# Kernel tuning notes

Measured on AMD Instinct MI355X. Metric: run time of the kernel, lower is better.

Reference implementation:

```python
import jax, jax.numpy as jnp
import numpy as np

VOCAB, INPUT, HIDDEN = 50000, 512, 1024
BATCH, MAX_LEN = 64, 256


def setup_inputs() -> dict:
    key = jax.random.key(0)
    ks = jax.random.split(key, 16)
    s = 0.02
    return {
        "last_output": jax.random.randint(ks[0], (BATCH,), 0, VOCAB),
        "last_hidden": jax.random.normal(ks[1], (BATCH, HIDDEN), jnp.float32),
        "encoder_outputs": jax.random.normal(ks[2], (MAX_LEN, BATCH, HIDDEN), jnp.float32),
        # embedding table (padding_idx=0 just means row 0 is a pad row; math is a plain gather)
        "embedding": jax.random.uniform(ks[3], (VOCAB, INPUT), jnp.float32, -0.25, 0.25),
        # concat attention: Linear(2H -> H) and v [H]
        "attn_W": jax.random.normal(ks[4], (HIDDEN, 2 * HIDDEN), jnp.float32) * s,
        "attn_b": jnp.zeros((HIDDEN,), jnp.float32),
        "v": jax.random.normal(ks[5], (HIDDEN,), jnp.float32) * s,
        # GRU (single layer): input size = INPUT + HIDDEN, gate order r,z,n (torch order)
        "W_ih": jax.random.normal(ks[6], (3 * HIDDEN, INPUT + HIDDEN), jnp.float32) * s,
        "W_hh": jax.random.uniform(ks[7], (3 * HIDDEN, HIDDEN), jnp.float32, -0.01, 0.01),
        "b_ih": jnp.zeros((3 * HIDDEN,), jnp.float32),
        "b_hh": jnp.zeros((3 * HIDDEN,), jnp.float32),
        # output projection Linear(2H -> vocab)
        "out_W": jax.random.normal(ks[8], (VOCAB, 2 * HIDDEN), jnp.float32) * s,
        "out_b": jnp.zeros((VOCAB,), jnp.float32),
    }


def reference(last_output, last_hidden, encoder_outputs, embedding,
              attn_W, attn_b, v, W_ih, W_hh, b_ih, b_hh, out_W, out_b):
    T, B, H = encoder_outputs.shape
    # --- embedding lookup: [B, INPUT]
    emb = embedding[last_output]

    # --- concat (Bahdanau-style, no tanh in original) attention, vectorized over T
    hid = jnp.broadcast_to(last_hidden[None], (T, B, H))
    cat = jnp.concatenate([hid, encoder_outputs], axis=-1)          # [T,B,2H]
    energy = jnp.einsum('tbk,hk->tbh', cat, attn_W) + attn_b        # [T,B,H]
    scores = jnp.einsum('tbh,h->bt', energy, v)                     # [B,T]
    attn = jax.nn.softmax(scores, axis=1)                           # [B,T]

    # --- context: [B,H]
    context = jnp.einsum('bt,tbh->bh', attn, encoder_outputs)

    # --- single GRU step (torch gate order r,z,n)
    x = jnp.concatenate([emb, context], axis=-1)                    # [B, INPUT+H]
    gi = x @ W_ih.T + b_ih                                          # [B,3H]
    gh = last_hidden @ W_hh.T + b_hh                                # [B,3H]
    i_r, i_z, i_n = jnp.split(gi, 3, axis=-1)
    h_r, h_z, h_n = jnp.split(gh, 3, axis=-1)
    r = jax.nn.sigmoid(i_r + h_r)
    z = jax.nn.sigmoid(i_z + h_z)
    n = jnp.tanh(i_n + r * h_n)
    h_new = (1.0 - z) * n + z * last_hidden                         # [B,H]

    # --- output projection + log_softmax over vocab
    logits = jnp.concatenate([h_new, context], axis=-1) @ out_W.T + out_b
    logp = jax.nn.log_softmax(logits, axis=-1)                      # [B,VOCAB]
    return logp, h_new
```

## Files before the change

### kernel.cpp

```cpp
#include <hip/hip_runtime.h>
#include <cstddef>

#define VOCAB  50000
#define INPUT  512
#define HIDDEN 1024
#define BATCH  64
#define MAXLEN 256
#define NBLK   1563

typedef float  f32x4 __attribute__((ext_vector_type(4)));
typedef __bf16 bf16x8 __attribute__((ext_vector_type(8)));

__device__ __forceinline__ bf16x8 cvt8(float4 a, float4 b) {
    bf16x8 r;
    r[0] = (__bf16)a.x; r[1] = (__bf16)a.y; r[2] = (__bf16)a.z; r[3] = (__bf16)a.w;
    r[4] = (__bf16)b.x; r[5] = (__bf16)b.y; r[6] = (__bf16)b.z; r[7] = (__bf16)b.w;
    return r;
}

__global__ void k_u2(const float* __restrict__ attn_W, const float* __restrict__ v,
                     float* __restrict__ u2) {
    int tid = threadIdx.x;
    int kk = blockIdx.x * 64 + (tid & 63);
    int hg = tid >> 6;
    float acc = 0.f;
#pragma unroll 8
    for (int h = hg * 256; h < hg * 256 + 256; ++h)
        acc += v[h] * attn_W[(size_t)h * (2 * HIDDEN) + HIDDEN + kk];
    __shared__ float red[4][64];
    red[hg][tid & 63] = acc;
    __syncthreads();
    if (tid < 64)
        u2[blockIdx.x * 64 + tid] = red[0][tid] + red[1][tid] + red[2][tid] + red[3][tid];
}

__global__ void k_scores_pack(const float* __restrict__ enc, const float* __restrict__ u2,
                              float* __restrict__ scores,
                              const int* __restrict__ last_output,
                              const float* __restrict__ embedding,
                              const float* __restrict__ hid,
                              __bf16* __restrict__ x_bf, __bf16* __restrict__ hid_bf) {
    int bid = blockIdx.x, tid = threadIdx.x;
    if (bid < 4096) {
        int wid = tid >> 6, lane = tid & 63;
        int p = bid * 4 + wid;
        const float* row = enc + (size_t)p * HIDDEN;
        float acc = 0.f;
#pragma unroll
        for (int i = 0; i < 4; ++i) {
            float4 e = *(const float4*)(row + lane * 4 + i * 256);
            float4 u = *(const float4*)(u2  + lane * 4 + i * 256);
            acc += e.x * u.x + e.y * u.y + e.z * u.z + e.w * u.w;
        }
#pragma unroll
        for (int off = 32; off; off >>= 1) acc += __shfl_down(acc, off, 64);
        if (lane == 0) scores[(p & 63) * MAXLEN + (p >> 6)] = acc;
    } else {
        int idx = (bid - 4096) * 256 + tid;
        if (idx < 64 * INPUT) {
            int b = idx >> 9, k = idx & 511;
            x_bf[b * 1536 + k] = (__bf16)embedding[(size_t)last_output[b] * INPUT + k];
        } else {
            idx -= 64 * INPUT;
            int b = idx >> 10, h = idx & 1023;
            hid_bf[b * HIDDEN + h] = (__bf16)hid[b * HIDDEN + h];
        }
    }
}

__global__ void k_ctx(const float* __restrict__ enc, const float* __restrict__ scores,
                      __bf16* __restrict__ x_bf, __bf16* __restrict__ y_bf) {
    int b = blockIdx.x >> 2, hc = blockIdx.x & 3, tid = threadIdx.x;
    __shared__ float a[256];
    __shared__ float red[256];
    float s = scores[b * MAXLEN + tid];
    red[tid] = s; __syncthreads();
    for (int off = 128; off; off >>= 1) { if (tid < off) red[tid] = fmaxf(red[tid], red[tid + off]); __syncthreads(); }
    float m = red[0]; __syncthreads();
    float e = expf(s - m);
    red[tid] = e; __syncthreads();
    for (int off = 128; off; off >>= 1) { if (tid < off) red[tid] += red[tid + off]; __syncthreads(); }
    a[tid] = e * (1.f / red[0]);
    __syncthreads();
    int h = hc * 256 + tid;
    float acc = 0.f;
#pragma unroll 8
    for (int t = 0; t < MAXLEN; ++t)
        acc += a[t] * enc[((size_t)(t * BATCH + b)) * HIDDEN + h];
    x_bf[b * 1536 + INPUT + h]   = (__bf16)acc;
    y_bf[b * 2048 + HIDDEN + h]  = (__bf16)acc;
}

__device__ __forceinline__ void gemm_tile(const float* __restrict__ W,
                                          const float* __restrict__ bias,
                                          const __bf16* __restrict__ A,
                                          float* __restrict__ out,
                                          int N, int K, int jt, int tid) {
    int wid = tid >> 6, lane = tid & 63;
    int j  = jt * 16 + (lane & 15);
    int kg = (lane >> 4) * 8;
    int kchunk = K >> 2;
    int kbeg = wid * kchunk, kend = kbeg + kchunk;
    const float*  wrow = W + (size_t)j * K;
    const __bf16* arow = A + (size_t)(lane & 15) * K;
    f32x4 acc[4] = {};
    for (int k0 = kbeg; k0 < kend; k0 += 32) {
        int kk = k0 + kg;
        float4 w0 = *(const float4*)(wrow + kk);
        float4 w1 = *(const float4*)(wrow + kk + 4);
        bf16x8 bw = cvt8(w0, w1);
#pragma unroll
        for (int mt = 0; mt < 4; ++mt) {
            bf16x8 av = *(const bf16x8*)(arow + (size_t)mt * 16 * K + kk);
            acc[mt] = __builtin_amdgcn_mfma_f32_16x16x32_bf16(av, bw, acc[mt], 0, 0, 0);
        }
    }
    __shared__ float lds[4][1024];
#pragma unroll
    for (int mt = 0; mt < 4; ++mt)
#pragma unroll
        for (int r = 0; r < 4; ++r) {
            int m = mt * 16 + (lane >> 4) * 4 + r;
            lds[wid][m * 16 + (lane & 15)] = acc[mt][r];
        }
    __syncthreads();
#pragma unroll
    for (int o = tid; o < 1024; o += 256) {
        float s = lds[0][o] + lds[1][o] + lds[2][o] + lds[3][o];
        int m = o >> 4, jl = o & 15;
        out[(size_t)m * N + jt * 16 + jl] = s + bias[jt * 16 + jl];
    }
}

__global__ __launch_bounds__(256) void k_gemm_gru(const float* __restrict__ W_ih,
                                                  const float* __restrict__ b_ih,
                                                  const __bf16* __restrict__ x_bf,
                                                  float* __restrict__ Gi,
                                                  const float* __restrict__ W_hh,
                                                  const float* __restrict__ b_hh,
                                                  const __bf16* __restrict__ hid_bf,
                                                  float* __restrict__ Gh) {
    int bid = blockIdx.x, tid = threadIdx.x;
    if (bid < 192) gemm_tile(W_ih, b_ih, x_bf,  Gi, 3072, 1536, bid,       tid);
    else           gemm_tile(W_hh, b_hh, hid_bf, Gh, 3072, 1024, bid - 192, tid);
}

__global__ void k_combine(const float* __restrict__ Gi, const float* __restrict__ Gh,
                          const float* __restrict__ hid, float* __restrict__ hnew_out,
                          __bf16* __restrict__ y_bf) {
    int idx = blockIdx.x * 256 + threadIdx.x;
    int b = idx >> 10, h = idx & 1023;
    const float* gi = Gi + (size_t)b * 3072;
    const float* gh = Gh + (size_t)b * 3072;
    float r  = 1.f / (1.f + expf(-(gi[h] + gh[h])));
    float z  = 1.f / (1.f + expf(-(gi[1024 + h] + gh[1024 + h])));
    float n  = tanhf(gi[2048 + h] + r * gh[2048 + h]);
    float hp = hid[b * HIDDEN + h];
    float hn = (1.f - z) * n + z * hp;
    hnew_out[b * HIDDEN + h] = hn;
    y_bf[b * 2048 + h] = (__bf16)hn;
}

__global__ __launch_bounds__(256) void k_gemv(const float* __restrict__ W,
                                              const float* __restrict__ bias,
                                              const __bf16* __restrict__ A,
                                              float* __restrict__ out,
                                              float* __restrict__ mw,
                                              float* __restrict__ sw) {
    int bid = blockIdx.x, tid = threadIdx.x;
    int wid = tid >> 6, lane = tid & 63;
    int kg = (lane >> 4) * 8;
    int kbeg = wid * 512, kend = kbeg + 512;
    int ntiles = (bid == NBLK - 1) ? 1 : 2;
    int j0 = bid * 32 + (lane & 15);
    int jr0 = min(j0,      VOCAB - 1);
    int jr1 = min(j0 + 16, VOCAB - 1);
    const float*  wrow0 = W + (size_t)jr0 * 2048;
    const float*  wrow1 = W + (size_t)jr1 * 2048;
    const __bf16* arow  = A + (size_t)(lane & 15) * 2048;
    f32x4 acc[2][4] = {};
    for (int k0 = kbeg; k0 < kend; k0 += 32) {
        int kk = k0 + kg;
        float4 p0 = *(const float4*)(wrow0 + kk);
        float4 p1 = *(const float4*)(wrow0 + kk + 4);
        float4 q0 = *(const float4*)(wrow1 + kk);
        float4 q1 = *(const float4*)(wrow1 + kk + 4);
        bf16x8 bw0 = cvt8(p0, p1);
        bf16x8 bw1 = cvt8(q0, q1);
#pragma unroll
        for (int mt = 0; mt < 4; ++mt) {
            bf16x8 av = *(const bf16x8*)(arow + (size_t)mt * 16 * 2048 + kk);
            acc[0][mt] = __builtin_amdgcn_mfma_f32_16x16x32_bf16(av, bw0, acc[0][mt], 0, 0, 0);
            acc[1][mt] = __builtin_amdgcn_mfma_f32_16x16x32_bf16(av, bw1, acc[1][mt], 0, 0, 0);
        }
    }
    __shared__ float lds[4][1024];
    float Mreg = -INFINITY, Sreg = 0.f;
    for (int u = 0; u < ntiles; ++u) {
        if (u) __syncthreads();
#pragma unroll
        for (int mt = 0; mt < 4; ++mt)
#pragma unroll
            for (int r = 0; r < 4; ++r) {
                int m = mt * 16 + (lane >> 4) * 4 + r;
                lds[wid][m * 16 + (lane & 15)] = acc[u][mt][r];
            }
        __syncthreads();
#pragma unroll
        for (int o = tid; o < 1024; o += 256) {
            float s = lds[0][o] + lds[1][o] + lds[2][o] + lds[3][o];
            int m = o >> 4, jl = o & 15;
            int jj = bid * 32 + u * 16 + jl;
            s += bias[jj];
            out[(size_t)m * VOCAB + jj] = s;
            lds[0][o] = s;
        }
        __syncthreads();
        if (tid < 64) {
            float mx = -INFINITY;
#pragma unroll
            for (int jl = 0; jl < 16; ++jl) mx = fmaxf(mx, lds[0][tid * 16 + jl]);
            float se = 0.f;
#pragma unroll
            for (int jl = 0; jl < 16; ++jl) se += expf(lds[0][tid * 16 + jl] - mx);
            float M2 = fmaxf(Mreg, mx);
            Sreg = Sreg * expf(Mreg - M2) + se * expf(mx - M2);
            Mreg = M2;
        }
    }
    if (tid < 64) {
        mw[(size_t)tid * NBLK + bid] = Mreg;
        sw[(size_t)tid * NBLK + bid] = Sreg;
    }
}

__global__ __launch_bounds__(256) void k_lse_fused(float* __restrict__ logits,
                                                   const float* __restrict__ mw,
                                                   const float* __restrict__ sw) {
    int bid = blockIdx.x, tid = threadIdx.x;
    int b = bid / 13, c = bid % 13;
    const float* mrow = mw + (size_t)b * NBLK;
    const float* srow = sw + (size_t)b * NBLK;
    __shared__ float red[256];
    float m = -INFINITY;
    for (int i = tid; i < NBLK; i += 256) m = fmaxf(m, mrow[i]);
    red[tid] = m; __syncthreads();
    for (int off = 128; off; off >>= 1) { if (tid < off) red[tid] = fmaxf(red[tid], red[tid + off]); __syncthreads(); }
    m = red[0]; __syncthreads();
    float s = 0.f;
    for (int i = tid; i < NBLK; i += 256) s += srow[i] * expf(mrow[i] - m);
    red[tid] = s; __syncthreads();
    for (int off = 128; off; off >>= 1) { if (tid < off) red[tid] += red[tid + off]; __syncthreads(); }
    float lse = m + logf(red[0]);
    int base = c * 4096;
    int len  = min(4096, VOCAB - base);
    float* row = logits + (size_t)b * VOCAB + base;
    for (int i = tid * 4; i < len; i += 1024) {
        float4 x = *(float4*)(row + i);
        x.x -= lse; x.y -= lse; x.z -= lse; x.w -= lse;
        *(float4*)(row + i) = x;
    }
}

extern "C" void kernel_launch(void* const* d_in, const int* in_sizes, int n_in,
                              void* d_out, int out_size, void* d_ws, size_t ws_size,
                              hipStream_t stream) {
    const int*   last_output = (const int*)  d_in[0];
    const float* last_hidden = (const float*)d_in[1];
    const float* enc         = (const float*)d_in[2];
    const float* embedding   = (const float*)d_in[3];
    const float* attn_W      = (const float*)d_in[4];
    const float* v           = (const float*)d_in[6];
    const float* W_ih        = (const float*)d_in[7];
    const float* W_hh        = (const float*)d_in[8];
    const float* b_ih        = (const float*)d_in[9];
    const float* b_hh        = (const float*)d_in[10];
    const float* out_W       = (const float*)d_in[11];
    const float* out_b       = (const float*)d_in[12];

    float* out_logp = (float*)d_out;
    float* out_hnew = (float*)d_out + (size_t)BATCH * VOCAB;

    char* ws = (char*)d_ws;
    float*  u2      = (float*) (ws + 0);
    float*  scores  = (float*) (ws + 4096);
    __bf16* x_bf    = (__bf16*)(ws + 69632);
    __bf16* hid_bf  = (__bf16*)(ws + 266240);
    __bf16* y_bf    = (__bf16*)(ws + 397312);
    float*  Gi      = (float*) (ws + 659456);
    float*  Gh      = (float*) (ws + 1445888);
    float*  mw      = (float*) (ws + 2232320);
    float*  sw      = (float*) (ws + 2636800);

    k_u2          <<<16,   256, 0, stream>>>(attn_W, v, u2);
    k_scores_pack <<<4480, 256, 0, stream>>>(enc, u2, scores, last_output, embedding,
                                             last_hidden, x_bf, hid_bf);
    k_ctx         <<<256,  256, 0, stream>>>(enc, scores, x_bf, y_bf);
    k_gemm_gru    <<<384,  256, 0, stream>>>(W_ih, b_ih, x_bf, Gi, W_hh, b_hh, hid_bf, Gh);
    k_combine     <<<256,  256, 0, stream>>>(Gi, Gh, last_hidden, out_hnew, y_bf);
    k_gemv        <<<NBLK, 256, 0, stream>>>(out_W, out_b, y_bf, out_logp, mw, sw);
    k_lse_fused   <<<832,  256, 0, stream>>>(out_logp, mw, sw);
}
```

Before: 214.4 us.

## Fuse attention scores, softmax and context into split-T flash-style kernel; narrow GEMV tiles

```diff
diff --git a/kernel.cpp b/kernel.cpp
--- a/kernel.cpp
+++ b/kernel.cpp
@@ -6,7 +6,7 @@
 #define HIDDEN 1024
 #define BATCH  64
 #define MAXLEN 256
-#define NBLK   1563
+#define NBLK   3125
 
 typedef float  f32x4 __attribute__((ext_vector_type(4)));
 typedef __bf16 bf16x8 __attribute__((ext_vector_type(8)));
@@ -18,77 +18,107 @@
     return r;
 }
 
-__global__ void k_u2(const float* __restrict__ attn_W, const float* __restrict__ v,
-                     float* __restrict__ u2) {
-    int tid = threadIdx.x;
-    int kk = blockIdx.x * 64 + (tid & 63);
-    int hg = tid >> 6;
+__device__ __forceinline__ bf16x8 cvt8v(f32x4 a, f32x4 b) {
+    bf16x8 r;
+    r[0] = (__bf16)a[0]; r[1] = (__bf16)a[1]; r[2] = (__bf16)a[2]; r[3] = (__bf16)a[3];
+    r[4] = (__bf16)b[0]; r[5] = (__bf16)b[1]; r[6] = (__bf16)b[2]; r[7] = (__bf16)b[3];
+    return r;
+}
+
+__global__ void k_u2_part(const float* __restrict__ attn_W, const float* __restrict__ v,
+                          float* __restrict__ u2p) {
+    int bid = blockIdx.x, tid = threadIdx.x;
+    int hq = bid >> 4, kc = bid & 15;
+    int kl = tid & 63, hg = tid >> 6;
+    int k = kc * 64 + kl;
     float acc = 0.f;
+    int h0 = hq * 256 + hg * 64;
 #pragma unroll 8
-    for (int h = hg * 256; h < hg * 256 + 256; ++h)
-        acc += v[h] * attn_W[(size_t)h * (2 * HIDDEN) + HIDDEN + kk];
+    for (int h = h0; h < h0 + 64; ++h)
+        acc += v[h] * attn_W[(size_t)h * (2 * HIDDEN) + HIDDEN + k];
     __shared__ float red[4][64];
-    red[hg][tid & 63] = acc;
+    red[hg][kl] = acc;
     __syncthreads();
     if (tid < 64)
-        u2[blockIdx.x * 64 + tid] = red[0][tid] + red[1][tid] + red[2][tid] + red[3][tid];
-}
-
-__global__ void k_scores_pack(const float* __restrict__ enc, const float* __restrict__ u2,
-                              float* __restrict__ scores,
-                              const int* __restrict__ last_output,
-                              const float* __restrict__ embedding,
-                              const float* __restrict__ hid,
-                              __bf16* __restrict__ x_bf, __bf16* __restrict__ hid_bf) {
-    int bid = blockIdx.x, tid = threadIdx.x;
-    if (bid < 4096) {
-        int wid = tid >> 6, lane = tid & 63;
-        int p = bid * 4 + wid;
-        const float* row = enc + (size_t)p * HIDDEN;
+        u2p[hq * 1024 + kc * 64 + tid] =
+            red[0][tid] + red[1][tid] + red[2][tid] + red[3][tid];
+}
+
+__global__ __launch_bounds__(256) void k_att(const float* __restrict__ enc,
+                                             const float* __restrict__ u2p,
+                                             float* __restrict__ mpart,
+                                             float* __restrict__ lpart,
+                                             float* __restrict__ ctxp) {
+    int bid = blockIdx.x, tid = threadIdx.x;
+    int b = bid >> 2, tq = bid & 3, t0 = tq * 64;
+    __shared__ float u2s[1024];
+    __shared__ float s_lds[64];
+    __shared__ float p_lds[64];
+    for (int i = tid; i < 1024; i += 256)
+        u2s[i] = u2p[i] + u2p[1024 + i] + u2p[2048 + i] + u2p[3072 + i];
+    __syncthreads();
+    int w = tid >> 6, lane = tid & 63;
+#pragma unroll 2
+    for (int it = 0; it < 16; ++it) {
+        int t = t0 + w * 16 + it;
+        const float* row = enc + ((size_t)t * BATCH + b) * HIDDEN;
         float acc = 0.f;
 #pragma unroll
         for (int i = 0; i < 4; ++i) {
             float4 e = *(const float4*)(row + lane * 4 + i * 256);
-            float4 u = *(const float4*)(u2  + lane * 4 + i * 256);
+            float4 u = *(const float4*)(&u2s[lane * 4 + i * 256]);
             acc += e.x * u.x + e.y * u.y + e.z * u.z + e.w * u.w;
         }
 #pragma unroll
         for (int off = 32; off; off >>= 1) acc += __shfl_down(acc, off, 64);
-        if (lane == 0) scores[(p & 63) * MAXLEN + (p >> 6)] = acc;
-    } else {
-        int idx = (bid - 4096) * 256 + tid;
-        if (idx < 64 * INPUT) {
-            int b = idx >> 9, k = idx & 511;
-            x_bf[b * 1536 + k] = (__bf16)embedding[(size_t)last_output[b] * INPUT + k];
-        } else {
-            idx -= 64 * INPUT;
-            int b = idx >> 10, h = idx & 1023;
-            hid_bf[b * HIDDEN + h] = (__bf16)hid[b * HIDDEN + h];
-        }
-    }
-}
-
-__global__ void k_ctx(const float* __restrict__ enc, const float* __restrict__ scores,
-                      __bf16* __restrict__ x_bf, __bf16* __restrict__ y_bf) {
+        if (lane == 0) s_lds[w * 16 + it] = acc;
+    }
+    __syncthreads();
+    float m = -INFINITY;
+#pragma unroll 8
+    for (int t = 0; t < 64; ++t) m = fmaxf(m, s_lds[t]);
+    if (tid < 64) p_lds[tid] = expf(s_lds[tid] - m);
+    __syncthreads();
+    float l = 0.f;
+#pragma unroll 8
+    for (int t = 0; t < 64; ++t) l += p_lds[t];
+    float4 acc = {0.f, 0.f, 0.f, 0.f};
+    const float* ebase = enc + ((size_t)t0 * BATCH + b) * HIDDEN + tid * 4;
+#pragma unroll 4
+    for (int t = 0; t < 64; ++t) {
+        float p = p_lds[t];
+        float4 e = *(const float4*)(ebase + (size_t)t * (BATCH * HIDDEN));
+        acc.x += p * e.x; acc.y += p * e.y; acc.z += p * e.z; acc.w += p * e.w;
+    }
+    int o = b * 4 + tq;
+    *(float4*)(ctxp + (size_t)o * 1024 + tid * 4) = acc;
+    if (tid == 0) { mpart[o] = m; lpart[o] = l; }
+}
+
+__global__ void k_att_comb(const float* __restrict__ mpart, const float* __restrict__ lpart,
+                           const float* __restrict__ ctxp,
+                           const int* __restrict__ last_output,
+                           const float* __restrict__ embedding,
+                           const float* __restrict__ hid,
+                           __bf16* __restrict__ x_bf, __bf16* __restrict__ hid_bf,
+                           __bf16* __restrict__ y_bf) {
     int b = blockIdx.x >> 2, hc = blockIdx.x & 3, tid = threadIdx.x;
-    __shared__ float a[256];
-    __shared__ float red[256];
-    float s = scores[b * MAXLEN + tid];
-    red[tid] = s; __syncthreads();
-    for (int off = 128; off; off >>= 1) { if (tid < off) red[tid] = fmaxf(red[tid], red[tid + off]); __syncthreads(); }
-    float m = red[0]; __syncthreads();
-    float e = expf(s - m);
-    red[tid] = e; __syncthreads();
-    for (int off = 128; off; off >>= 1) { if (tid < off) red[tid] += red[tid + off]; __syncthreads(); }
-    a[tid] = e * (1.f / red[0]);
-    __syncthreads();
+    float m0 = mpart[b * 4 + 0], m1 = mpart[b * 4 + 1];
+    float m2 = mpart[b * 4 + 2], m3 = mpart[b * 4 + 3];
+    float M = fmaxf(fmaxf(m0, m1), fmaxf(m2, m3));
+    float w0 = expf(m0 - M), w1 = expf(m1 - M), w2 = expf(m2 - M), w3 = expf(m3 - M);
+    float denom = lpart[b * 4 + 0] * w0 + lpart[b * 4 + 1] * w1 +
+                  lpart[b * 4 + 2] * w2 + lpart[b * 4 + 3] * w3;
+    float inv = 1.f / denom;
     int h = hc * 256 + tid;
-    float acc = 0.f;
-#pragma unroll 8
-    for (int t = 0; t < MAXLEN; ++t)
-        acc += a[t] * enc[((size_t)(t * BATCH + b)) * HIDDEN + h];
-    x_bf[b * 1536 + INPUT + h]   = (__bf16)acc;
-    y_bf[b * 2048 + HIDDEN + h]  = (__bf16)acc;
+    const float* cp = ctxp + (size_t)b * 4096 + h;
+    float c = (w0 * cp[0] + w1 * cp[1024] + w2 * cp[2048] + w3 * cp[3072]) * inv;
+    x_bf[b * 1536 + INPUT + h]  = (__bf16)c;
+    y_bf[b * 2048 + HIDDEN + h] = (__bf16)c;
+    if (hc < 2)
+        x_bf[b * 1536 + hc * 256 + tid] =
+            (__bf16)embedding[(size_t)last_output[b] * INPUT + hc * 256 + tid];
+    hid_bf[b * HIDDEN + hc * 256 + tid] = (__bf16)hid[b * HIDDEN + hc * 256 + tid];
 }
 
 __device__ __forceinline__ void gemm_tile(const float* __restrict__ W,
@@ -170,67 +200,51 @@
     int bid = blockIdx.x, tid = threadIdx.x;
     int wid = tid >> 6, lane = tid & 63;
     int kg = (lane >> 4) * 8;
-    int kbeg = wid * 512, kend = kbeg + 512;
-    int ntiles = (bid == NBLK - 1) ? 1 : 2;
-    int j0 = bid * 32 + (lane & 15);
-    int jr0 = min(j0,      VOCAB - 1);
-    int jr1 = min(j0 + 16, VOCAB - 1);
-    const float*  wrow0 = W + (size_t)jr0 * 2048;
-    const float*  wrow1 = W + (size_t)jr1 * 2048;
-    const __bf16* arow  = A + (size_t)(lane & 15) * 2048;
-    f32x4 acc[2][4] = {};
-    for (int k0 = kbeg; k0 < kend; k0 += 32) {
+    int kbeg = wid * 512;
+    int j = bid * 16 + (lane & 15);
+    const float*  wrow = W + (size_t)j * 2048;
+    const __bf16* arow = A + (size_t)(lane & 15) * 2048;
+    f32x4 acc[4] = {};
+    for (int k0 = kbeg; k0 < kbeg + 512; k0 += 32) {
         int kk = k0 + kg;
-        float4 p0 = *(const float4*)(wrow0 + kk);
-        float4 p1 = *(const float4*)(wrow0 + kk + 4);
-        float4 q0 = *(const float4*)(wrow1 + kk);
-        float4 q1 = *(const float4*)(wrow1 + kk + 4);
-        bf16x8 bw0 = cvt8(p0, p1);
-        bf16x8 bw1 = cvt8(q0, q1);
+        const f32x4* wp = (const f32x4*)(wrow + kk);
+        f32x4 w0 = __builtin_nontemporal_load(wp);
+        f32x4 w1 = __builtin_nontemporal_load(wp + 1);
+        bf16x8 bw = cvt8v(w0, w1);
 #pragma unroll
         for (int mt = 0; mt < 4; ++mt) {
             bf16x8 av = *(const bf16x8*)(arow + (size_t)mt * 16 * 2048 + kk);
-            acc[0][mt] = __builtin_amdgcn_mfma_f32_16x16x32_bf16(av, bw0, acc[0][mt], 0, 0, 0);
-            acc[1][mt] = __builtin_amdgcn_mfma_f32_16x16x32_bf16(av, bw1, acc[1][mt], 0, 0, 0);
+            acc[mt] = __builtin_amdgcn_mfma_f32_16x16x32_bf16(av, bw, acc[mt], 0, 0, 0);
         }
     }
     __shared__ float lds[4][1024];
-    float Mreg = -INFINITY, Sreg = 0.f;
-    for (int u = 0; u < ntiles; ++u) {
-        if (u) __syncthreads();
-#pragma unroll
-        for (int mt = 0; mt < 4; ++mt)
-#pragma unroll
-            for (int r = 0; r < 4; ++r) {
-                int m = mt * 16 + (lane >> 4) * 4 + r;
-                lds[wid][m * 16 + (lane & 15)] = acc[u][mt][r];
-            }
-        __syncthreads();
-#pragma unroll
-        for (int o = tid; o < 1024; o += 256) {
-            float s = lds[0][o] + lds[1][o] + lds[2][o] + lds[3][o];
-            int m = o >> 4, jl = o & 15;
-            int jj = bid * 32 + u * 16 + jl;
-            s += bias[jj];
-            out[(size_t)m * VOCAB + jj] = s;
-            lds[0][o] = s;
-        }
-        __syncthreads();
-        if (tid < 64) {
-            float mx = -INFINITY;
-#pragma unroll
-            for (int jl = 0; jl < 16; ++jl) mx = fmaxf(mx, lds[0][tid * 16 + jl]);
-            float se = 0.f;
-#pragma unroll
-            for (int jl = 0; jl < 16; ++jl) se += expf(lds[0][tid * 16 + jl] - mx);
-            float M2 = fmaxf(Mreg, mx);
-            Sreg = Sreg * expf(Mreg - M2) + se * expf(mx - M2);
-            Mreg = M2;
-        }
-    }
+#pragma unroll
+    for (int mt = 0; mt < 4; ++mt)
+#pragma unroll
+        for (int r = 0; r < 4; ++r) {
+            int m = mt * 16 + (lane >> 4) * 4 + r;
+            lds[wid][m * 16 + (lane & 15)] = acc[mt][r];
+        }
+    __syncthreads();
+#pragma unroll
+    for (int o = tid; o < 1024; o += 256) {
+        float s = lds[0][o] + lds[1][o] + lds[2][o] + lds[3][o];
+        int m = o >> 4, jl = o & 15;
+        int jj = bid * 16 + jl;
+        s += bias[jj];
+        out[(size_t)m * VOCAB + jj] = s;
+        lds[0][o] = s;
+    }
+    __syncthreads();
     if (tid < 64) {
-        mw[(size_t)tid * NBLK + bid] = Mreg;
-        sw[(size_t)tid * NBLK + bid] = Sreg;
+        float mx = -INFINITY;
+#pragma unroll
+        for (int jl = 0; jl < 16; ++jl) mx = fmaxf(mx, lds[0][tid * 16 + jl]);
+        float se = 0.f;
+#pragma unroll
+        for (int jl = 0; jl < 16; ++jl) se += expf(lds[0][tid * 16 + jl] - mx);
+        mw[(size_t)tid * NBLK + bid] = mx;
+        sw[(size_t)tid * NBLK + bid] = se;
     }
 }
 
@@ -282,22 +296,24 @@
     float* out_hnew = (float*)d_out + (size_t)BATCH * VOCAB;
 
     char* ws = (char*)d_ws;
-    float*  u2      = (float*) (ws + 0);
-    float*  scores  = (float*) (ws + 4096);
-    __bf16* x_bf    = (__bf16*)(ws + 69632);
-    __bf16* hid_bf  = (__bf16*)(ws + 266240);
-    __bf16* y_bf    = (__bf16*)(ws + 397312);
-    float*  Gi      = (float*) (ws + 659456);
-    float*  Gh      = (float*) (ws + 1445888);
-    float*  mw      = (float*) (ws + 2232320);
-    float*  sw      = (float*) (ws + 2636800);
-
-    k_u2          <<<16,   256, 0, stream>>>(attn_W, v, u2);
-    k_scores_pack <<<4480, 256, 0, stream>>>(enc, u2, scores, last_output, embedding,
-                                             last_hidden, x_bf, hid_bf);
-    k_ctx         <<<256,  256, 0, stream>>>(enc, scores, x_bf, y_bf);
-    k_gemm_gru    <<<384,  256, 0, stream>>>(W_ih, b_ih, x_bf, Gi, W_hh, b_hh, hid_bf, Gh);
-    k_combine     <<<256,  256, 0, stream>>>(Gi, Gh, last_hidden, out_hnew, y_bf);
-    k_gemv        <<<NBLK, 256, 0, stream>>>(out_W, out_b, y_bf, out_logp, mw, sw);
-    k_lse_fused   <<<832,  256, 0, stream>>>(out_logp, mw, sw);
-}
+    float*  u2p     = (float*) (ws + 0);
+    float*  mpart   = (float*) (ws + 16384);
+    float*  lpart   = (float*) (ws + 17408);
+    float*  ctxp    = (float*) (ws + 18432);
+    __bf16* x_bf    = (__bf16*)(ws + 1067008);
+    __bf16* hid_bf  = (__bf16*)(ws + 1263616);
+    __bf16* y_bf    = (__bf16*)(ws + 1394688);
+    float*  Gi      = (float*) (ws + 1656832);
+    float*  Gh      = (float*) (ws + 2443264);
+    float*  mw      = (float*) (ws + 3229696);
+    float*  sw      = (float*) (ws + 4029696);
+
+    k_u2_part  <<<64,   256, 0, stream>>>(attn_W, v, u2p);
+    k_att      <<<256,  256, 0, stream>>>(enc, u2p, mpart, lpart, ctxp);
+    k_att_comb <<<256,  256, 0, stream>>>(mpart, lpart, ctxp, last_output, embedding,
+                                          last_hidden, x_bf, hid_bf, y_bf);
+    k_gemm_gru <<<384,  256, 0, stream>>>(W_ih, b_ih, x_bf, Gi, W_hh, b_hh, hid_bf, Gh);
+    k_combine  <<<256,  256, 0, stream>>>(Gi, Gh, last_hidden, out_hnew, y_bf);
+    k_gemv     <<<NBLK, 256, 0, stream>>>(out_W, out_b, y_bf, out_logp, mw, sw);
+    k_lse_fused<<<832,  256, 0, stream>>>(out_logp, mw, sw);
+}
```

Result: slower. 243.3 us (+13.5%).

## Fuse attention score computation into context kernel and merge u2 with packing

Applied to the files above, without the earlier changes.

```diff
diff --git a/kernel.cpp b/kernel.cpp
--- a/kernel.cpp
+++ b/kernel.cpp
@@ -18,45 +18,30 @@
     return r;
 }
 
-__global__ void k_u2(const float* __restrict__ attn_W, const float* __restrict__ v,
-                     float* __restrict__ u2) {
-    int tid = threadIdx.x;
-    int kk = blockIdx.x * 64 + (tid & 63);
-    int hg = tid >> 6;
-    float acc = 0.f;
+__global__ void k_u2_pack(const float* __restrict__ attn_W, const float* __restrict__ v,
+                          float* __restrict__ u2p,
+                          const int* __restrict__ last_output,
+                          const float* __restrict__ embedding,
+                          const float* __restrict__ hid,
+                          __bf16* __restrict__ x_bf, __bf16* __restrict__ hid_bf) {
+    int bid = blockIdx.x, tid = threadIdx.x;
+    if (bid < 64) {
+        int hq = bid >> 4, kc = bid & 15;
+        int kl = tid & 63, hg = tid >> 6;
+        int k = kc * 64 + kl;
+        float acc = 0.f;
+        int h0 = hq * 256 + hg * 64;
 #pragma unroll 8
-    for (int h = hg * 256; h < hg * 256 + 256; ++h)
-        acc += v[h] * attn_W[(size_t)h * (2 * HIDDEN) + HIDDEN + kk];
-    __shared__ float red[4][64];
-    red[hg][tid & 63] = acc;
-    __syncthreads();
-    if (tid < 64)
-        u2[blockIdx.x * 64 + tid] = red[0][tid] + red[1][tid] + red[2][tid] + red[3][tid];
-}
-
-__global__ void k_scores_pack(const float* __restrict__ enc, const float* __restrict__ u2,
-                              float* __restrict__ scores,
-                              const int* __restrict__ last_output,
-                              const float* __restrict__ embedding,
-                              const float* __restrict__ hid,
-                              __bf16* __restrict__ x_bf, __bf16* __restrict__ hid_bf) {
-    int bid = blockIdx.x, tid = threadIdx.x;
-    if (bid < 4096) {
-        int wid = tid >> 6, lane = tid & 63;
-        int p = bid * 4 + wid;
-        const float* row = enc + (size_t)p * HIDDEN;
-        float acc = 0.f;
-#pragma unroll
-        for (int i = 0; i < 4; ++i) {
-            float4 e = *(const float4*)(row + lane * 4 + i * 256);
-            float4 u = *(const float4*)(u2  + lane * 4 + i * 256);
-            acc += e.x * u.x + e.y * u.y + e.z * u.z + e.w * u.w;
-        }
-#pragma unroll
-        for (int off = 32; off; off >>= 1) acc += __shfl_down(acc, off, 64);
-        if (lane == 0) scores[(p & 63) * MAXLEN + (p >> 6)] = acc;
+        for (int h = h0; h < h0 + 64; ++h)
+            acc += v[h] * attn_W[(size_t)h * (2 * HIDDEN) + HIDDEN + k];
+        __shared__ float red[4][64];
+        red[hg][kl] = acc;
+        __syncthreads();
+        if (tid < 64)
+            u2p[hq * 1024 + kc * 64 + tid] =
+                red[0][tid] + red[1][tid] + red[2][tid] + red[3][tid];
     } else {
-        int idx = (bid - 4096) * 256 + tid;
+        int idx = (bid - 64) * 256 + tid;
         if (idx < 64 * INPUT) {
             int b = idx >> 9, k = idx & 511;
             x_bf[b * 1536 + k] = (__bf16)embedding[(size_t)last_output[b] * INPUT + k];
@@ -68,27 +53,51 @@
     }
 }
 
-__global__ void k_ctx(const float* __restrict__ enc, const float* __restrict__ scores,
-                      __bf16* __restrict__ x_bf, __bf16* __restrict__ y_bf) {
-    int b = blockIdx.x >> 2, hc = blockIdx.x & 3, tid = threadIdx.x;
-    __shared__ float a[256];
+__global__ __launch_bounds__(256) void k_att_full(const float* __restrict__ enc,
+                                                  const float* __restrict__ u2p,
+                                                  __bf16* __restrict__ x_bf,
+                                                  __bf16* __restrict__ y_bf) {
+    int bid = blockIdx.x, tid = threadIdx.x;
+    int b = bid >> 2, hc = bid & 3;
+    __shared__ float u2s[1024];
+    __shared__ float s_lds[256];
     __shared__ float red[256];
-    float s = scores[b * MAXLEN + tid];
-    red[tid] = s; __syncthreads();
+    for (int i = tid; i < 1024; i += 256)
+        u2s[i] = u2p[i] + u2p[1024 + i] + u2p[2048 + i] + u2p[3072 + i];
+    __syncthreads();
+    int w = tid >> 6, lane = tid & 63;
+#pragma unroll 4
+    for (int it = 0; it < 64; ++it) {
+        int t = w * 64 + it;
+        const float* row = enc + ((size_t)t * BATCH + b) * HIDDEN;
+        float acc = 0.f;
+#pragma unroll
+        for (int i = 0; i < 4; ++i) {
+            float4 e = *(const float4*)(row + lane * 4 + i * 256);
+            float4 u = *(const float4*)(&u2s[lane * 4 + i * 256]);
+            acc += e.x * u.x + e.y * u.y + e.z * u.z + e.w * u.w;
+        }
+#pragma unroll
+        for (int off = 32; off; off >>= 1) acc += __shfl_down(acc, off, 64);
+        if (lane == 0) s_lds[t] = acc;
+    }
+    __syncthreads();
+    float sv = s_lds[tid];
+    red[tid] = sv; __syncthreads();
     for (int off = 128; off; off >>= 1) { if (tid < off) red[tid] = fmaxf(red[tid], red[tid + off]); __syncthreads(); }
     float m = red[0]; __syncthreads();
-    float e = expf(s - m);
+    float e = expf(sv - m);
     red[tid] = e; __syncthreads();
     for (int off = 128; off; off >>= 1) { if (tid < off) red[tid] += red[tid + off]; __syncthreads(); }
-    a[tid] = e * (1.f / red[0]);
+    s_lds[tid] = e * (1.f / red[0]);
     __syncthreads();
     int h = hc * 256 + tid;
     float acc = 0.f;
 #pragma unroll 8
     for (int t = 0; t < MAXLEN; ++t)
-        acc += a[t] * enc[((size_t)(t * BATCH + b)) * HIDDEN + h];
-    x_bf[b * 1536 + INPUT + h]   = (__bf16)acc;
-    y_bf[b * 2048 + HIDDEN + h]  = (__bf16)acc;
+        acc += s_lds[t] * enc[((size_t)(t * BATCH + b)) * HIDDEN + h];
+    x_bf[b * 1536 + INPUT + h]  = (__bf16)acc;
+    y_bf[b * 2048 + HIDDEN + h] = (__bf16)acc;
 }
 
 __device__ __forceinline__ void gemm_tile(const float* __restrict__ W,
@@ -282,22 +291,20 @@
     float* out_hnew = (float*)d_out + (size_t)BATCH * VOCAB;
 
     char* ws = (char*)d_ws;
-    float*  u2      = (float*) (ws + 0);
-    float*  scores  = (float*) (ws + 4096);
-    __bf16* x_bf    = (__bf16*)(ws + 69632);
-    __bf16* hid_bf  = (__bf16*)(ws + 266240);
-    __bf16* y_bf    = (__bf16*)(ws + 397312);
-    float*  Gi      = (float*) (ws + 659456);
-    float*  Gh      = (float*) (ws + 1445888);
-    float*  mw      = (float*) (ws + 2232320);
-    float*  sw      = (float*) (ws + 2636800);
-
-    k_u2          <<<16,   256, 0, stream>>>(attn_W, v, u2);
-    k_scores_pack <<<4480, 256, 0, stream>>>(enc, u2, scores, last_output, embedding,
-                                             last_hidden, x_bf, hid_bf);
-    k_ctx         <<<256,  256, 0, stream>>>(enc, scores, x_bf, y_bf);
-    k_gemm_gru    <<<384,  256, 0, stream>>>(W_ih, b_ih, x_bf, Gi, W_hh, b_hh, hid_bf, Gh);
-    k_combine     <<<256,  256, 0, stream>>>(Gi, Gh, last_hidden, out_hnew, y_bf);
-    k_gemv        <<<NBLK, 256, 0, stream>>>(out_W, out_b, y_bf, out_logp, mw, sw);
-    k_lse_fused   <<<832,  256, 0, stream>>>(out_logp, mw, sw);
-}
+    float*  u2p     = (float*) (ws + 0);
+    __bf16* x_bf    = (__bf16*)(ws + 16384);
+    __bf16* hid_bf  = (__bf16*)(ws + 212992);
+    __bf16* y_bf    = (__bf16*)(ws + 344064);
+    float*  Gi      = (float*) (ws + 606208);
+    float*  Gh      = (float*) (ws + 1392640);
+    float*  mw      = (float*) (ws + 2179072);
+    float*  sw      = (float*) (ws + 2579072);
+
+    k_u2_pack  <<<448,  256, 0, stream>>>(attn_W, v, u2p, last_output, embedding,
+                                          last_hidden, x_bf, hid_bf);
+    k_att_full <<<256,  256, 0, stream>>>(enc, u2p, x_bf, y_bf);
+    k_gemm_gru <<<384,  256, 0, stream>>>(W_ih, b_ih, x_bf, Gi, W_hh, b_hh, hid_bf, Gh);
+    k_combine  <<<256,  256, 0, stream>>>(Gi, Gh, last_hidden, out_hnew, y_bf);
+    k_gemv     <<<NBLK, 256, 0, stream>>>(out_W, out_b, y_bf, out_logp, mw, sw);
+    k_lse_fused<<<832,  256, 0, stream>>>(out_logp, mw, sw);
+}
```

Measured after the change: 245.4 us. 1.14x slower.
